# Optimization experiments

Measured on AMD Instinct MI355X. Metric: run time of the kernel, lower is better.

The kernel has to match this reference:

```python
import jax, jax.numpy as jnp
import numpy as np

C = 256
NUM_HEADS = 8
GROUPS = 8
EPS = 1e-5


def setup_inputs() -> dict:
    key = jax.random.key(0)
    ks = jax.random.split(key, 7)
    B, H, W = 2, 64, 64
    x = jax.random.normal(ks[0], (B, C, H, W), dtype=jnp.float32)
    gn_weight = jnp.ones((C,), dtype=jnp.float32)
    gn_bias = jnp.zeros((C,), dtype=jnp.float32)
    # 1x1 convs == per-pixel linear layers
    w_qkv = jax.random.normal(ks[1], (3 * C, C), dtype=jnp.float32) * (1.0 / np.sqrt(C))
    b_qkv = jax.random.normal(ks[2], (3 * C,), dtype=jnp.float32) * 0.01
    w_proj = jax.random.normal(ks[3], (C, C), dtype=jnp.float32) * (1.0 / np.sqrt(C))
    b_proj = jax.random.normal(ks[4], (C,), dtype=jnp.float32) * 0.01
    return {"x": x, "gn_weight": gn_weight, "gn_bias": gn_bias,
            "w_qkv": w_qkv, "b_qkv": b_qkv, "w_proj": w_proj, "b_proj": b_proj}


def reference(x, gn_weight, gn_bias, w_qkv, b_qkv, w_proj, b_proj):
    B, Cc, H, W = x.shape
    nh = NUM_HEADS
    hd = Cc // nh
    N = H * W
    scale = hd ** (-0.5)

    # GroupNorm(8, C): normalize over (C/G, H, W) per group, biased variance
    xg = x.reshape(B, GROUPS, Cc // GROUPS, H, W)
    mean = xg.mean(axis=(2, 3, 4), keepdims=True)
    var = xg.var(axis=(2, 3, 4), keepdims=True)
    hn = (xg - mean) * jax.lax.rsqrt(var + EPS)
    hn = hn.reshape(B, Cc, H, W) * gn_weight[None, :, None, None] + gn_bias[None, :, None, None]

    hf = hn.reshape(B, Cc, N)                       # [B, C, N]
    qkv = jnp.einsum('oc,bcn->bon', w_qkv, hf) + b_qkv[None, :, None]  # [B, 3C, N]
    qkv = qkv.reshape(B, 3, nh, hd, N)
    # q,k,v: [B, nh, N, hd]
    q = jnp.transpose(qkv[:, 0], (0, 1, 3, 2))
    k = jnp.transpose(qkv[:, 1], (0, 1, 3, 2))
    v = jnp.transpose(qkv[:, 2], (0, 1, 3, 2))

    attn = jnp.einsum('bhqd,bhkd->bhqk', q, k) * scale  # [B, nh, N, N]
    attn = jax.nn.softmax(attn, axis=-1)
    o = jnp.einsum('bhqk,bhkd->bhqd', attn, v)           # [B, nh, N, hd]
    o = jnp.transpose(o, (0, 1, 3, 2)).reshape(B, Cc, H, W)

    of = o.reshape(B, Cc, N)
    out = jnp.einsum('oc,bcn->bon', w_proj, of) + b_proj[None, :, None]
    return out.reshape(B, Cc, H, W)
```

## Files before the change

### kernel.cpp

```cpp
#include <hip/hip_runtime.h>


typedef _Float16 half8 __attribute__((ext_vector_type(8)));
typedef _Float16 half4 __attribute__((ext_vector_type(4)));
typedef __fp16   fp16x2 __attribute__((ext_vector_type(2)));
typedef float    f32x4 __attribute__((ext_vector_type(4)));
typedef int      int2v __attribute__((ext_vector_type(2)));

__device__ __forceinline__ f32x4 mfma16(half8 a, half8 b, f32x4 c) {
  return __builtin_amdgcn_mfma_f32_16x16x32_f16(a, b, c, 0, 0, 0);
}
__device__ __forceinline__ f32x4 mfma16k16(half4 a, half4 b, f32x4 c) {
  return __builtin_amdgcn_mfma_f32_16x16x16f16(a, b, c, 0, 0, 0);
}

#if __has_builtin(__builtin_amdgcn_exp2f)
#define EXP2(x) __builtin_amdgcn_exp2f(x)
#else
#define EXP2(x) exp2f(x)
#endif

__device__ __forceinline__ unsigned short h_bits(_Float16 h) {
  return __builtin_bit_cast(unsigned short, h);
}
__device__ __forceinline__ int h2_bits(fp16x2 h) {
  return __builtin_bit_cast(int, h);
}

constexpr float CSCALE = (float)(1.4426950408889634 / 5.656854249492381);
constexpr float LOSC   = 2048.0f;
constexpr float ILOSC  = 1.0f / 2048.0f;

__global__ __launch_bounds__(256) void gn_stats(const float* __restrict__ x,
                                                float* __restrict__ stats) {
  const int bg = blockIdx.x, ch = blockIdx.y, tid = threadIdx.x;
  const float* p = x + (size_t)bg * 131072 + (size_t)ch * 4096;
  float s = 0.f, ss = 0.f;
#pragma unroll
  for (int j = 0; j < 4; ++j) {
    f32x4 v = *(const f32x4*)(p + j * 1024 + tid * 4);
#pragma unroll
    for (int k = 0; k < 4; ++k) { s += v[k]; ss += v[k] * v[k]; }
  }
#pragma unroll
  for (int m = 1; m <= 32; m <<= 1) { s += __shfl_xor(s, m); ss += __shfl_xor(ss, m); }
  __shared__ float red[8];
  const int wv = tid >> 6;
  if ((tid & 63) == 0) { red[wv * 2] = s; red[wv * 2 + 1] = ss; }
  __syncthreads();
  if (tid == 0) {
    float S = red[0] + red[2] + red[4] + red[6];
    float SS = red[1] + red[3] + red[5] + red[7];
    atomicAdd(&stats[bg * 2], S);
    atomicAdd(&stats[bg * 2 + 1], SS);
  }
}

__global__ __launch_bounds__(256) void gn_apply(const float* __restrict__ x,
                                                const float* __restrict__ gw,
                                                const float* __restrict__ gb,
                                                const float* __restrict__ stats,
                                                _Float16* __restrict__ hn_hi,
                                                _Float16* __restrict__ hn_lo) {
  __shared__ float tile[64 * 65];
  const int tid = threadIdx.x;
  const int a = tid & 15;
  const int row16 = tid >> 4;
  const int b = blockIdx.z, c0 = blockIdx.y * 64, n0 = blockIdx.x * 64;
#pragma unroll
  for (int m = 0; m < 4; ++m) {
    const int cl = row16 + 16 * m;
    const int c = c0 + cl;
    const int g = c >> 5;
    const float s = stats[(b * 8 + g) * 2];
    const float ss = stats[(b * 8 + g) * 2 + 1];
    const float mean = s * (1.f / 131072.f);
    const float var = ss * (1.f / 131072.f) - mean * mean;
    const float rstd = rsqrtf(var + 1e-5f);
    const float ga = gw[c] * rstd;
    const float be = gb[c] - mean * ga;
    f32x4 xv = *(const f32x4*)(x + ((size_t)(b * 256 + c)) * 4096 + n0 + a * 4);
#pragma unroll
    for (int j = 0; j < 4; ++j) tile[cl * 65 + a * 4 + j] = xv[j] * ga + be;
  }
  __syncthreads();
#pragma unroll
  for (int m = 0; m < 4; ++m) {
    const int nl = row16 + 16 * m;
    const int cb = a * 4;
    unsigned short hh[4], ll[4];
#pragma unroll
    for (int j = 0; j < 4; ++j) {
      float v = tile[(cb + j) * 65 + nl];
      _Float16 h = (_Float16)v;
      hh[j] = h_bits(h);
      ll[j] = h_bits((_Float16)((v - (float)h) * LOSC));
    }
    int2v uh, ul;
    uh[0] = hh[0] | (hh[1] << 16); uh[1] = hh[2] | (hh[3] << 16);
    ul[0] = ll[0] | (ll[1] << 16); ul[1] = ll[2] | (ll[3] << 16);
    size_t off = ((size_t)(b * 4096 + n0 + nl)) * 256 + c0 + cb;
    *(int2v*)(hn_hi + off) = uh;
    *(int2v*)(hn_lo + off) = ul;
  }
}

__global__ __launch_bounds__(256) void wsplit(const float* __restrict__ wq,
                                              const float* __restrict__ wp,
                                              _Float16* __restrict__ wqh,
                                              _Float16* __restrict__ wql,
                                              _Float16* __restrict__ wph,
                                              _Float16* __restrict__ wpl) {
  const int idx = blockIdx.x * 256 + threadIdx.x;
  if (idx < 196608) {
    float v = wq[idx];
    _Float16 h = (_Float16)v;
    wqh[idx] = h;
    wql[idx] = (_Float16)((v - (float)h) * LOSC);
  } else {
    const int i2 = idx - 196608;
    float v = wp[i2];
    _Float16 h = (_Float16)v;
    wph[i2] = h;
    wpl[i2] = (_Float16)((v - (float)h) * LOSC);
  }
}

template <int MODE>
__global__ __launch_bounds__(256) void gemm_split(
    const _Float16* __restrict__ Ahi, const _Float16* __restrict__ Alo,
    const _Float16* __restrict__ Bhi, const _Float16* __restrict__ Blo,
    const float* __restrict__ bias,
    _Float16* __restrict__ qkT, _Float16* __restrict__ v_t,
    float* __restrict__ outp) {
  __shared__ _Float16 a_lds[8192];
  __shared__ _Float16 b_lds[8192];
  const int tid = threadIdx.x, lane = tid & 63, wv = tid >> 6;
  const int qq = lane >> 4, ii = lane & 15;
  const int m0 = blockIdx.x * 64, n0 = blockIdx.y * 64, bz = blockIdx.z;
  const int hlT = (tid >> 7) & 1, cT = (tid >> 6) & 1;
  const int qT = (tid >> 4) & 3, iT = tid & 15;
  const _Float16* Asel = hlT ? Alo : Ahi;
  const _Float16* Bsel = hlT ? Blo : Bhi;
  const _Float16* aptr = Asel + (size_t)(m0 + iT) * 256 + 32 * cT + 8 * qT;
  const _Float16* bptr = Bsel + ((size_t)(bz * 4096 + n0 + iT)) * 256 + 32 * cT + 8 * qT;

  f32x4 acc[4] = {}, acc2[4] = {};
  for (int k0 = 0; k0 < 256; k0 += 64) {
#pragma unroll
    for (int j = 0; j < 4; ++j) {
      *(half8*)(a_lds + (((j * 2 + hlT) * 2 + cT) * 64 + (tid & 63)) * 8) =
          *(const half8*)(aptr + (size_t)(16 * j) * 256 + k0);
      *(half8*)(b_lds + (((j * 2 + hlT) * 2 + cT) * 64 + (tid & 63)) * 8) =
          *(const half8*)(bptr + (size_t)(16 * j) * 256 + k0);
    }
    __syncthreads();
    half8 ah[2], al[2];
#pragma unroll
    for (int c = 0; c < 2; ++c) {
      ah[c] = *(const half8*)(a_lds + (((wv * 2 + 0) * 2 + c) * 64 + lane) * 8);
      al[c] = *(const half8*)(a_lds + (((wv * 2 + 1) * 2 + c) * 64 + lane) * 8);
    }
#pragma unroll
    for (int t = 0; t < 4; ++t) {
#pragma unroll
      for (int c = 0; c < 2; ++c) {
        half8 bh_ = *(const half8*)(b_lds + (((t * 2 + 0) * 2 + c) * 64 + lane) * 8);
        half8 bl_ = *(const half8*)(b_lds + (((t * 2 + 1) * 2 + c) * 64 + lane) * 8);
        acc[t]  = mfma16(ah[c], bh_, acc[t]);
        acc2[t] = mfma16(ah[c], bl_, acc2[t]);
        acc2[t] = mfma16(al[c], bh_, acc2[t]);
      }
    }
    __syncthreads();
  }

  const int och0 = m0 + 16 * wv + 4 * qq;
  if (MODE == 0) {
    if (m0 < 512) {
      const float sc = (m0 < 256) ? CSCALE : 1.0f;
#pragma unroll
      for (int t = 0; t < 4; ++t) {
        const int n = n0 + 16 * t + ii;
        unsigned short hh[4];
#pragma unroll
        for (int r = 0; r < 4; ++r) {
          float val = (acc[t][r] + acc2[t][r] * ILOSC + bias[och0 + r]) * sc;
          hh[r] = h_bits((_Float16)val);
        }
        int2v u;
        u[0] = hh[0] | (hh[1] << 16);
        u[1] = hh[2] | (hh[3] << 16);
        *(int2v*)(qkT + ((size_t)(bz * 4096 + n)) * 512 + och0) = u;
      }
    } else {
#pragma unroll
      for (int t = 0; t < 4; ++t) {
#pragma unroll
        for (int r = 0; r < 4; ++r) {
          const int och = och0 + r;
          const int d = och - 512;
          const int hd_ = d & 31, head = d >> 5;
          const int n = n0 + 16 * t + ii;
          float val = acc[t][r] + acc2[t][r] * ILOSC + bias[och];
          v_t[((size_t)((bz * 8 + head) * 32 + hd_)) * 4096 + n] = (_Float16)val;
        }
      }
    }
  } else {
#pragma unroll
    for (int t = 0; t < 4; ++t) {
#pragma unroll
      for (int r = 0; r < 4; ++r) {
        const int och = och0 + r;
        const int n = n0 + 16 * t + ii;
        outp[((size_t)(bz * 256 + och)) * 4096 + n] =
            acc[t][r] + acc2[t][r] * ILOSC + bias[och];
      }
    }
  }
}

__global__ __launch_bounds__(512) void attn_kernel(
    const _Float16* __restrict__ qkT, const _Float16* __restrict__ v_t,
    _Float16* __restrict__ o_hi, _Float16* __restrict__ o_lo) {
  __shared__ _Float16 k_lds[2][128 * 40];
  __shared__ _Float16 v_lds[2][32 * 136];
  const int tid = threadIdx.x, lane = tid & 63, wv = tid >> 6;
  const int qq = lane >> 4, ii = lane & 15;
  const int bh = blockIdx.y, b = bh >> 3, h = bh & 7;
  const int n0 = blockIdx.x * 128;

  half8 qf = *(const half8*)(qkT + ((size_t)(b * 4096 + n0 + 16 * wv + ii)) * 512 +
                             h * 32 + 8 * qq);

  const int kkey = tid >> 2, kq = tid & 3;
  const _Float16* ksrc = qkT + ((size_t)(b * 4096 + kkey)) * 512 + 256 + h * 32 + 8 * kq;
  const int kdst = kkey * 40 + 8 * kq;
  const int vd = tid >> 4, vc = tid & 15;
  const _Float16* vsrc = v_t + ((size_t)(bh * 32 + vd)) * 4096 + 8 * vc;
  const int vdst = vd * 136 + 8 * vc;

  half4 onesf;
#pragma unroll
  for (int j = 0; j < 4; ++j) onesf[j] = (_Float16)1.0f;

  f32x4 o0 = {}, o1 = {}, accl = {};

  half8 kreg = *(const half8*)ksrc;
  half8 vreg = *(const half8*)vsrc;
  *(half8*)(k_lds[0] + kdst) = kreg;
  *(half8*)(v_lds[0] + vdst) = vreg;
  __syncthreads();

  for (int kb = 0; kb < 32; ++kb) {
    const int cur = kb & 1;
    if (kb < 31) {
      kreg = *(const half8*)(ksrc + (size_t)(kb + 1) * 128 * 512);
      vreg = *(const half8*)(vsrc + (size_t)(kb + 1) * 128);
    }
    const _Float16* kbase = k_lds[cur];
    const _Float16* vbase = v_lds[cur];

#pragma unroll
    for (int t = 0; t < 8; ++t) {
      half8 kf = *(const half8*)(kbase + (16 * t + ii) * 40 + 8 * qq);
      f32x4 z = {};
      f32x4 st = mfma16(kf, qf, z);
      fp16x2 e01 = __builtin_amdgcn_cvt_pkrtz(EXP2(st[0]), EXP2(st[1]));
      fp16x2 e23 = __builtin_amdgcn_cvt_pkrtz(EXP2(st[2]), EXP2(st[3]));
      int2v pi;
      pi[0] = h2_bits(e01);
      pi[1] = h2_bits(e23);
      half4 pt = __builtin_bit_cast(half4, pi);
      half4 vf0 = *(const half4*)(vbase + ii * 136 + 16 * t + 4 * qq);
      half4 vf1 = *(const half4*)(vbase + (16 + ii) * 136 + 16 * t + 4 * qq);
      o0 = mfma16k16(vf0, pt, o0);
      o1 = mfma16k16(vf1, pt, o1);
      accl = mfma16k16(onesf, pt, accl);
    }

    if (kb < 31) {
      _Float16* knext = k_lds[cur ^ 1];
      _Float16* vnext = v_lds[cur ^ 1];
      *(half8*)(knext + kdst) = kreg;
      *(half8*)(vnext + vdst) = vreg;
    }
    __syncthreads();
  }

  const float inv = 1.0f / accl[0];
  const size_t row = ((size_t)(b * 4096 + n0 + 16 * wv + ii)) * 256 + h * 32;
  unsigned short hh[4], ll[4];
#pragma unroll
  for (int r = 0; r < 4; ++r) {
    float v = o0[r] * inv;
    _Float16 hv = (_Float16)v;
    hh[r] = h_bits(hv);
    ll[r] = h_bits((_Float16)((v - (float)hv) * LOSC));
  }
  int2v uh, ul;
  uh[0] = hh[0] | (hh[1] << 16); uh[1] = hh[2] | (hh[3] << 16);
  ul[0] = ll[0] | (ll[1] << 16); ul[1] = ll[2] | (ll[3] << 16);
  *(int2v*)(o_hi + row + 4 * qq) = uh;
  *(int2v*)(o_lo + row + 4 * qq) = ul;
#pragma unroll
  for (int r = 0; r < 4; ++r) {
    float v = o1[r] * inv;
    _Float16 hv = (_Float16)v;
    hh[r] = h_bits(hv);
    ll[r] = h_bits((_Float16)((v - (float)hv) * LOSC));
  }
  uh[0] = hh[0] | (hh[1] << 16); uh[1] = hh[2] | (hh[3] << 16);
  ul[0] = ll[0] | (ll[1] << 16); ul[1] = ll[2] | (ll[3] << 16);
  *(int2v*)(o_hi + row + 16 + 4 * qq) = uh;
  *(int2v*)(o_lo + row + 16 + 4 * qq) = ul;
}

extern "C" void kernel_launch(void* const* d_in, const int* in_sizes, int n_in,
                              void* d_out, int out_size, void* d_ws, size_t ws_size,
                              hipStream_t stream) {
  const float* x     = (const float*)d_in[0];
  const float* gnw   = (const float*)d_in[1];
  const float* gnb   = (const float*)d_in[2];
  const float* wqkv  = (const float*)d_in[3];
  const float* bqkv  = (const float*)d_in[4];
  const float* wproj = (const float*)d_in[5];
  const float* bproj = (const float*)d_in[6];
  float* out = (float*)d_out;

  char* ws = (char*)d_ws;
  size_t off = 0;
  auto alloc = [&](size_t bytes) -> char* {
    char* p = ws + off;
    off += (bytes + 255) & ~(size_t)255;
    return p;
  };
  float*    stats  = (float*)alloc(128);
  _Float16* hn_hi  = (_Float16*)alloc((size_t)2 * 4096 * 256 * 2);
  _Float16* hn_lo  = (_Float16*)alloc((size_t)2 * 4096 * 256 * 2);
  _Float16* wq_hi  = (_Float16*)alloc((size_t)768 * 256 * 2);
  _Float16* wq_lo  = (_Float16*)alloc((size_t)768 * 256 * 2);
  _Float16* wp_hi  = (_Float16*)alloc((size_t)256 * 256 * 2);
  _Float16* wp_lo  = (_Float16*)alloc((size_t)256 * 256 * 2);
  _Float16* qkT    = (_Float16*)alloc((size_t)2 * 4096 * 512 * 2);
  _Float16* v_t    = (_Float16*)alloc((size_t)16 * 32 * 4096 * 2);
  _Float16* o_hi   = (_Float16*)alloc((size_t)2 * 4096 * 256 * 2);
  _Float16* o_lo   = (_Float16*)alloc((size_t)2 * 4096 * 256 * 2);
  if (off > ws_size) return;

  (void)hipMemsetAsync(stats, 0, 256, stream);
  gn_stats<<<dim3(16, 32), 256, 0, stream>>>(x, stats);
  gn_apply<<<dim3(64, 4, 2), 256, 0, stream>>>(x, gnw, gnb, stats, hn_hi, hn_lo);
  wsplit<<<1024, 256, 0, stream>>>(wqkv, wproj, wq_hi, wq_lo, wp_hi, wp_lo);
  gemm_split<0><<<dim3(12, 64, 2), 256, 0, stream>>>(wq_hi, wq_lo, hn_hi, hn_lo,
                                                     bqkv, qkT, v_t, nullptr);
  attn_kernel<<<dim3(32, 16), 512, 0, stream>>>(qkT, v_t, o_hi, o_lo);
  gemm_split<1><<<dim3(4, 64, 2), 256, 0, stream>>>(wp_hi, wp_lo, o_hi, o_lo,
                                                    bproj, nullptr, nullptr, out);
}
```

Before: 182.4 us.

## Process two query tiles per wave in attention and use K=32 PV MFMA

The attention kernel now runs 256 threads, with each wave handling 32 queries (two 16-row Q fragments) instead of 16. This reuses every K and V fragment read from LDS across both query tiles. The key rows are permuted when loaded into LDS so that the 16x16x32 score output can feed the P·V product directly through the 16x16x32 MFMA, replacing the 16x16x16 variant and halving the PV and normaliser instruction count. The cost is more registers per wave, fewer waves per block, and twice the global loads per thread when filling LDS.

```diff
diff --git a/kernel.cpp b/kernel.cpp
--- a/kernel.cpp
+++ b/kernel.cpp
@@ -2,16 +2,13 @@
 
 
 typedef _Float16 half8 __attribute__((ext_vector_type(8)));
-typedef _Float16 half4 __attribute__((ext_vector_type(4)));
 typedef __fp16   fp16x2 __attribute__((ext_vector_type(2)));
 typedef float    f32x4 __attribute__((ext_vector_type(4)));
 typedef int      int2v __attribute__((ext_vector_type(2)));
+typedef int      int4v __attribute__((ext_vector_type(4)));
 
 __device__ __forceinline__ f32x4 mfma16(half8 a, half8 b, f32x4 c) {
   return __builtin_amdgcn_mfma_f32_16x16x32_f16(a, b, c, 0, 0, 0);
-}
-__device__ __forceinline__ f32x4 mfma16k16(half4 a, half4 b, f32x4 c) {
-  return __builtin_amdgcn_mfma_f32_16x16x16f16(a, b, c, 0, 0, 0);
 }
 
 #if __has_builtin(__builtin_amdgcn_exp2f)
@@ -221,7 +218,7 @@
   }
 }
 
-__global__ __launch_bounds__(512) void attn_kernel(
+__global__ __launch_bounds__(256) void attn_kernel(
     const _Float16* __restrict__ qkT, const _Float16* __restrict__ v_t,
     _Float16* __restrict__ o_hi, _Float16* __restrict__ o_lo) {
   __shared__ _Float16 k_lds[2][128 * 40];
@@ -231,90 +228,130 @@
   const int bh = blockIdx.y, b = bh >> 3, h = bh & 7;
   const int n0 = blockIdx.x * 128;
 
-  half8 qf = *(const half8*)(qkT + ((size_t)(b * 4096 + n0 + 16 * wv + ii)) * 512 +
-                             h * 32 + 8 * qq);
-
-  const int kkey = tid >> 2, kq = tid & 3;
-  const _Float16* ksrc = qkT + ((size_t)(b * 4096 + kkey)) * 512 + 256 + h * 32 + 8 * kq;
-  const int kdst = kkey * 40 + 8 * kq;
-  const int vd = tid >> 4, vc = tid & 15;
-  const _Float16* vsrc = v_t + ((size_t)(bh * 32 + vd)) * 4096 + 8 * vc;
-  const int vdst = vd * 136 + 8 * vc;
-
-  half4 onesf;
-#pragma unroll
-  for (int j = 0; j < 4; ++j) onesf[j] = (_Float16)1.0f;
-
-  f32x4 o0 = {}, o1 = {}, accl = {};
-
-  half8 kreg = *(const half8*)ksrc;
-  half8 vreg = *(const half8*)vsrc;
-  *(half8*)(k_lds[0] + kdst) = kreg;
-  *(half8*)(v_lds[0] + vdst) = vreg;
+  const _Float16* qbase =
+      qkT + ((size_t)(b * 4096 + n0 + 32 * wv + ii)) * 512 + h * 32 + 8 * qq;
+  half8 qf0 = *(const half8*)qbase;
+  half8 qf1 = *(const half8*)(qbase + (size_t)16 * 512);
+
+  const _Float16* ksrc[2];
+  int kdst[2];
+  const _Float16* vsrc[2];
+  int vdst[2];
+#pragma unroll
+  for (int rep = 0; rep < 2; ++rep) {
+    const int idx = tid + 256 * rep;
+    const int slot = idx >> 2, kq = idx & 3;
+    const int tau = slot >> 4, m = slot & 15;
+    const int g = 32 * (tau >> 1) + 4 * (tau & 1) + 8 * (m >> 2) + (m & 3);
+    ksrc[rep] = qkT + ((size_t)(b * 4096 + g)) * 512 + 256 + h * 32 + 8 * kq;
+    kdst[rep] = slot * 40 + 8 * kq;
+    const int d = idx >> 4, vc = idx & 15;
+    vsrc[rep] = v_t + ((size_t)(bh * 32 + d)) * 4096 + 8 * vc;
+    vdst[rep] = d * 136 + 8 * vc;
+  }
+
+  half8 ones8;
+#pragma unroll
+  for (int j = 0; j < 8; ++j) ones8[j] = (_Float16)1.0f;
+
+  f32x4 o00 = {}, o10 = {}, o01 = {}, o11 = {}, accl0 = {}, accl1 = {};
+
+  half8 kr0 = *(const half8*)ksrc[0];
+  half8 kr1 = *(const half8*)ksrc[1];
+  half8 vr0 = *(const half8*)vsrc[0];
+  half8 vr1 = *(const half8*)vsrc[1];
+  *(half8*)(k_lds[0] + kdst[0]) = kr0;
+  *(half8*)(k_lds[0] + kdst[1]) = kr1;
+  *(half8*)(v_lds[0] + vdst[0]) = vr0;
+  *(half8*)(v_lds[0] + vdst[1]) = vr1;
   __syncthreads();
 
   for (int kb = 0; kb < 32; ++kb) {
     const int cur = kb & 1;
     if (kb < 31) {
-      kreg = *(const half8*)(ksrc + (size_t)(kb + 1) * 128 * 512);
-      vreg = *(const half8*)(vsrc + (size_t)(kb + 1) * 128);
+      const size_t ko = (size_t)(kb + 1) * 128 * 512;
+      const size_t vo = (size_t)(kb + 1) * 128;
+      kr0 = *(const half8*)(ksrc[0] + ko);
+      kr1 = *(const half8*)(ksrc[1] + ko);
+      vr0 = *(const half8*)(vsrc[0] + vo);
+      vr1 = *(const half8*)(vsrc[1] + vo);
     }
     const _Float16* kbase = k_lds[cur];
     const _Float16* vbase = v_lds[cur];
 
 #pragma unroll
-    for (int t = 0; t < 8; ++t) {
-      half8 kf = *(const half8*)(kbase + (16 * t + ii) * 40 + 8 * qq);
+    for (int u = 0; u < 4; ++u) {
+      half8 kfa = *(const half8*)(kbase + (32 * u + ii) * 40 + 8 * qq);
+      half8 kfb = *(const half8*)(kbase + (32 * u + 16 + ii) * 40 + 8 * qq);
       f32x4 z = {};
-      f32x4 st = mfma16(kf, qf, z);
-      fp16x2 e01 = __builtin_amdgcn_cvt_pkrtz(EXP2(st[0]), EXP2(st[1]));
-      fp16x2 e23 = __builtin_amdgcn_cvt_pkrtz(EXP2(st[2]), EXP2(st[3]));
-      int2v pi;
-      pi[0] = h2_bits(e01);
-      pi[1] = h2_bits(e23);
-      half4 pt = __builtin_bit_cast(half4, pi);
-      half4 vf0 = *(const half4*)(vbase + ii * 136 + 16 * t + 4 * qq);
-      half4 vf1 = *(const half4*)(vbase + (16 + ii) * 136 + 16 * t + 4 * qq);
-      o0 = mfma16k16(vf0, pt, o0);
-      o1 = mfma16k16(vf1, pt, o1);
-      accl = mfma16k16(onesf, pt, accl);
+      f32x4 sa0 = mfma16(kfa, qf0, z);
+      f32x4 sb0 = mfma16(kfb, qf0, z);
+      f32x4 sa1 = mfma16(kfa, qf1, z);
+      f32x4 sb1 = mfma16(kfb, qf1, z);
+      int4v p0, p1;
+      p0[0] = h2_bits(__builtin_amdgcn_cvt_pkrtz(EXP2(sa0[0]), EXP2(sa0[1])));
+      p0[1] = h2_bits(__builtin_amdgcn_cvt_pkrtz(EXP2(sa0[2]), EXP2(sa0[3])));
+      p0[2] = h2_bits(__builtin_amdgcn_cvt_pkrtz(EXP2(sb0[0]), EXP2(sb0[1])));
+      p0[3] = h2_bits(__builtin_amdgcn_cvt_pkrtz(EXP2(sb0[2]), EXP2(sb0[3])));
+      p1[0] = h2_bits(__builtin_amdgcn_cvt_pkrtz(EXP2(sa1[0]), EXP2(sa1[1])));
+      p1[1] = h2_bits(__builtin_amdgcn_cvt_pkrtz(EXP2(sa1[2]), EXP2(sa1[3])));
+      p1[2] = h2_bits(__builtin_amdgcn_cvt_pkrtz(EXP2(sb1[0]), EXP2(sb1[1])));
+      p1[3] = h2_bits(__builtin_amdgcn_cvt_pkrtz(EXP2(sb1[2]), EXP2(sb1[3])));
+      half8 pt0 = __builtin_bit_cast(half8, p0);
+      half8 pt1 = __builtin_bit_cast(half8, p1);
+      half8 vf0 = *(const half8*)(vbase + ii * 136 + 32 * u + 8 * qq);
+      half8 vf1 = *(const half8*)(vbase + (16 + ii) * 136 + 32 * u + 8 * qq);
+      o00 = mfma16(vf0, pt0, o00);
+      o10 = mfma16(vf1, pt0, o10);
+      accl0 = mfma16(ones8, pt0, accl0);
+      o01 = mfma16(vf0, pt1, o01);
+      o11 = mfma16(vf1, pt1, o11);
+      accl1 = mfma16(ones8, pt1, accl1);
     }
 
     if (kb < 31) {
-      _Float16* knext = k_lds[cur ^ 1];
-      _Float16* vnext = v_lds[cur ^ 1];
-      *(half8*)(knext + kdst) = kreg;
-      *(half8*)(vnext + vdst) = vreg;
+      _Float16* kn = k_lds[cur ^ 1];
+      _Float16* vn = v_lds[cur ^ 1];
+      *(half8*)(kn + kdst[0]) = kr0;
+      *(half8*)(kn + kdst[1]) = kr1;
+      *(half8*)(vn + vdst[0]) = vr0;
+      *(half8*)(vn + vdst[1]) = vr1;
     }
     __syncthreads();
   }
 
-  const float inv = 1.0f / accl[0];
-  const size_t row = ((size_t)(b * 4096 + n0 + 16 * wv + ii)) * 256 + h * 32;
-  unsigned short hh[4], ll[4];
-#pragma unroll
-  for (int r = 0; r < 4; ++r) {
-    float v = o0[r] * inv;
-    _Float16 hv = (_Float16)v;
-    hh[r] = h_bits(hv);
-    ll[r] = h_bits((_Float16)((v - (float)hv) * LOSC));
-  }
-  int2v uh, ul;
-  uh[0] = hh[0] | (hh[1] << 16); uh[1] = hh[2] | (hh[3] << 16);
-  ul[0] = ll[0] | (ll[1] << 16); ul[1] = ll[2] | (ll[3] << 16);
-  *(int2v*)(o_hi + row + 4 * qq) = uh;
-  *(int2v*)(o_lo + row + 4 * qq) = ul;
-#pragma unroll
-  for (int r = 0; r < 4; ++r) {
-    float v = o1[r] * inv;
-    _Float16 hv = (_Float16)v;
-    hh[r] = h_bits(hv);
-    ll[r] = h_bits((_Float16)((v - (float)hv) * LOSC));
-  }
-  uh[0] = hh[0] | (hh[1] << 16); uh[1] = hh[2] | (hh[3] << 16);
-  ul[0] = ll[0] | (ll[1] << 16); ul[1] = ll[2] | (ll[3] << 16);
-  *(int2v*)(o_hi + row + 16 + 4 * qq) = uh;
-  *(int2v*)(o_lo + row + 16 + 4 * qq) = ul;
+#pragma unroll
+  for (int hf = 0; hf < 2; ++hf) {
+    const f32x4& oa = hf ? o01 : o00;
+    const f32x4& ob = hf ? o11 : o10;
+    const float inv = 1.0f / (hf ? accl1[0] : accl0[0]);
+    const size_t row =
+        ((size_t)(b * 4096 + n0 + 32 * wv + 16 * hf + ii)) * 256 + h * 32;
+    unsigned short hh[4], ll[4];
+#pragma unroll
+    for (int r = 0; r < 4; ++r) {
+      float v = oa[r] * inv;
+      _Float16 hv = (_Float16)v;
+      hh[r] = h_bits(hv);
+      ll[r] = h_bits((_Float16)((v - (float)hv) * LOSC));
+    }
+    int2v uh, ul;
+    uh[0] = hh[0] | (hh[1] << 16); uh[1] = hh[2] | (hh[3] << 16);
+    ul[0] = ll[0] | (ll[1] << 16); ul[1] = ll[2] | (ll[3] << 16);
+    *(int2v*)(o_hi + row + 4 * qq) = uh;
+    *(int2v*)(o_lo + row + 4 * qq) = ul;
+#pragma unroll
+    for (int r = 0; r < 4; ++r) {
+      float v = ob[r] * inv;
+      _Float16 hv = (_Float16)v;
+      hh[r] = h_bits(hv);
+      ll[r] = h_bits((_Float16)((v - (float)hv) * LOSC));
+    }
+    uh[0] = hh[0] | (hh[1] << 16); uh[1] = hh[2] | (hh[3] << 16);
+    ul[0] = ll[0] | (ll[1] << 16); ul[1] = ll[2] | (ll[3] << 16);
+    *(int2v*)(o_hi + row + 16 + 4 * qq) = uh;
+    *(int2v*)(o_lo + row + 16 + 4 * qq) = ul;
+  }
 }
 
 extern "C" void kernel_launch(void* const* d_in, const int* in_sizes, int n_in,
@@ -355,7 +392,7 @@
   wsplit<<<1024, 256, 0, stream>>>(wqkv, wproj, wq_hi, wq_lo, wp_hi, wp_lo);
   gemm_split<0><<<dim3(12, 64, 2), 256, 0, stream>>>(wq_hi, wq_lo, hn_hi, hn_lo,
                                                      bqkv, qkT, v_t, nullptr);
-  attn_kernel<<<dim3(32, 16), 512, 0, stream>>>(qkT, v_t, o_hi, o_lo);
+  attn_kernel<<<dim3(32, 16), 256, 0, stream>>>(qkT, v_t, o_hi, o_lo);
   gemm_split<1><<<dim3(4, 64, 2), 256, 0, stream>>>(wp_hi, wp_lo, o_hi, o_lo,
                                                     bproj, nullptr, nullptr, out);
 }
```

Measured after the change: 179.0 us. About the same (-1.8%).
